# Kernel tuning notes

Hardware: AMD Instinct MI355X
Metric: run time of the kernel (lower is better)

The kernel has to match this reference:

```python
import jax, jax.numpy as jnp
import numpy as np

B, C, H, W = 8, 128, 256, 256
WS = 8          # window_size (square)
HEADS = 4


def setup_inputs() -> dict:
    key = jax.random.key(0)
    k1, k2, k3, k4 = jax.random.split(key, 4)
    x = jax.random.normal(k1, (B, C, H, W), dtype=jnp.float32)
    # 1x1 convs are per-pixel matmuls; store weights as [out, in]
    w_qkv = jax.random.normal(k2, (3 * C, C), dtype=jnp.float32) * 0.05   # qkv conv, bias=False
    w_proj = jax.random.normal(k3, (C, C), dtype=jnp.float32) * 0.05      # proj conv weight
    b_proj = jax.random.normal(k4, (C,), dtype=jnp.float32) * 0.01        # proj conv bias
    return {"x": x, "w_qkv": w_qkv, "w_proj": w_proj, "b_proj": b_proj}


def reference(x, w_qkv, w_proj, b_proj):
    b, c, h, w = x.shape
    ws, heads = WS, HEADS
    d = c // heads
    scale = d ** -0.5
    hn, wn = h // ws, w // ws
    n = ws * ws  # tokens per window

    # unfold with kernel=stride=ws -> row-major window partition
    # [B,C,H,W] -> [B*hn*wn, C, n]
    xw = x.reshape(b, c, hn, ws, wn, ws)
    xw = xw.transpose(0, 2, 4, 1, 3, 5).reshape(b * hn * wn, c, n)

    # 1x1 conv QKV projection (no bias)
    qkv = jnp.einsum('oc,bcn->bon', w_qkv, xw)  # [Bw, 3C, n]
    q, k, v = jnp.split(qkv, 3, axis=1)
    q = q.reshape(-1, heads, d, n)
    k = k.reshape(-1, heads, d, n)
    v = v.reshape(-1, heads, d, n)

    # attn = (q^T k) * scale, softmax over keys
    attn = jax.nn.softmax(jnp.einsum('bhdn,bhdm->bhnm', q, k) * scale, axis=-1)
    out = jnp.einsum('bhnm,bhdm->bhdn', attn, v).reshape(-1, c, n)  # [Bw, C, n]

    # 1x1 proj conv with bias
    out = jnp.einsum('oc,bcn->bon', w_proj, out) + b_proj[None, :, None]

    # fold windows back: [Bw, C, n] -> [B, C, H, W]
    out = out.reshape(b, hn, wn, c, ws, ws)
    out = out.transpose(0, 3, 1, 4, 2, 5).reshape(b, c, h, w)
    return out
```

## Files before the change

### kernel.cpp

```cpp
#include <hip/hip_runtime.h>


#define HH    256
#define WWID  256
#define SCALE 0.17677669529663687f
#define LOG2E 1.44269504088896340736f

typedef float  f32x4  __attribute__((ext_vector_type(4)));
typedef __bf16 bf16x8 __attribute__((ext_vector_type(8)));
typedef __bf16 bf16x4 __attribute__((ext_vector_type(4)));
typedef __bf16 bf16x2 __attribute__((ext_vector_type(2)));

#define SCR_BASE 16384

__global__ void prep_weights(const float* __restrict__ wqkv,
                             const float* __restrict__ wproj,
                             __bf16* __restrict__ wbf) {
  int i = blockIdx.x * 256 + threadIdx.x;
  float v = (i < 49152) ? wqkv[i] : wproj[i - 49152];
  if (i < 16384) v *= SCALE * LOG2E;
  wbf[i] = (__bf16)v;
}

__global__ __launch_bounds__(256, 2)
void winattn_main(const float* __restrict__ x,
                  const __bf16* __restrict__ wqkv,
                  const __bf16* __restrict__ wproj,
                  const float* __restrict__ bproj,
                  float* __restrict__ out) {
  __shared__ __align__(16) char smem[32768];

  const int tid  = threadIdx.x;
  const int lane = tid & 63;
  const int wv   = tid >> 6;
  const int l15  = lane & 15;
  const int l4   = lane >> 4;

  const int bid = blockIdx.x;
  const int win = ((bid & 7) << 10) | (bid >> 3);
  const int b   = win >> 10;
  const int wy  = (win >> 5) & 31;
  const int wx  = win & 31;
  const int gy0 = wy * 8, gx0 = wx * 8;

  #pragma unroll
  for (int it = 0; it < 4; ++it) {
    int idx   = tid + it * 256;
    int cpair = idx >> 4;
    int r     = idx & 15;
    int ty    = r >> 1, tx4 = r & 1;
    const float* px = x + (((size_t)(b * 128 + 2 * cpair) * HH + gy0 + ty) * WWID + gx0 + tx4 * 4);
    float4 v0 = *(const float4*)px;
    float4 v1 = *(const float4*)(px + (size_t)HH * WWID);
    float a0[4] = {v0.x, v0.y, v0.z, v0.w};
    float a1[4] = {v1.x, v1.y, v1.z, v1.w};
    #pragma unroll
    for (int i = 0; i < 4; ++i) {
      int tok = ty * 8 + tx4 * 4 + i;
      bf16x2 w2 = {(__bf16)a0[i], (__bf16)a1[i]};
      int byte = (tok * 256 + cpair * 4) ^ ((tok & 15) << 4);
      *(bf16x2*)(smem + byte) = w2;
    }
  }
  __syncthreads();

  const int scr = SCR_BASE + wv * 4096;
  bf16x8 bk[4], aq[4], bv[2][2];

  #define XT_AFRAG(mt, kt) \
    (*(const bf16x8*)(smem + ((((mt) * 16 + l15) * 256 + ((kt) * 32 + l4 * 8) * 2) ^ \
                              ((((mt) * 16 + l15) & 15) << 4))))

  {
    f32x4 accQ[2][4] = {}, accK[2][4] = {};
    __builtin_amdgcn_s_setprio(1);
    #pragma unroll
    for (int kt = 0; kt < 4; ++kt) {
      bf16x8 xf[4];
      #pragma unroll
      for (int mt = 0; mt < 4; ++mt) xf[mt] = XT_AFRAG(mt, kt);
      #pragma unroll
      for (int nt2 = 0; nt2 < 2; ++nt2) {
        bf16x8 wq = *(const bf16x8*)(wqkv + (size_t)(wv * 32 + nt2 * 16 + l15) * 128 + kt * 32 + l4 * 8);
        bf16x8 wk = *(const bf16x8*)(wqkv + (size_t)(128 + wv * 32 + nt2 * 16 + l15) * 128 + kt * 32 + l4 * 8);
        #pragma unroll
        for (int mt = 0; mt < 4; ++mt) {
          accQ[nt2][mt] = __builtin_amdgcn_mfma_f32_16x16x32_bf16(wq, xf[mt], accQ[nt2][mt], 0, 0, 0);
          accK[nt2][mt] = __builtin_amdgcn_mfma_f32_16x16x32_bf16(wk, xf[mt], accK[nt2][mt], 0, 0, 0);
        }
      }
    }
    __builtin_amdgcn_s_setprio(0);
    #pragma unroll
    for (int nt2 = 0; nt2 < 2; ++nt2)
      #pragma unroll
      for (int mt = 0; mt < 4; ++mt) {
        int tok = mt * 16 + l15;
        bf16x4 kp = {(__bf16)accK[nt2][mt][0], (__bf16)accK[nt2][mt][1],
                     (__bf16)accK[nt2][mt][2], (__bf16)accK[nt2][mt][3]};
        int byte = scr + ((tok * 64 + (nt2 * 16 + l4 * 4) * 2) ^ ((tok & 3) << 4));
        *(bf16x4*)(smem + byte) = kp;
      }
    #pragma unroll
    for (int mtS = 0; mtS < 4; ++mtS) {
      int m    = mtS * 16 + l15;
      int byte = scr + ((m * 64 + l4 * 16) ^ ((m & 3) << 4));
      bk[mtS] = *(const bf16x8*)(smem + byte);
    }
    #pragma unroll
    for (int nt2 = 0; nt2 < 2; ++nt2)
      #pragma unroll
      for (int mt = 0; mt < 4; ++mt) {
        int tok = mt * 16 + l15;
        bf16x4 qp = {(__bf16)accQ[nt2][mt][0], (__bf16)accQ[nt2][mt][1],
                     (__bf16)accQ[nt2][mt][2], (__bf16)accQ[nt2][mt][3]};
        int byte = scr + ((tok * 64 + (nt2 * 16 + l4 * 4) * 2) ^ ((tok & 3) << 4));
        *(bf16x4*)(smem + byte) = qp;
      }
    #pragma unroll
    for (int t = 0; t < 4; ++t) {
      int tok  = t * 16 + l15;
      int byte = scr + ((tok * 64 + l4 * 16) ^ ((tok & 3) << 4));
      aq[t] = *(const bf16x8*)(smem + byte);
    }
  }

  {
    f32x4 accV[2][4] = {};
    __builtin_amdgcn_s_setprio(1);
    #pragma unroll
    for (int kt = 0; kt < 4; ++kt) {
      bf16x8 xf[4];
      #pragma unroll
      for (int mt = 0; mt < 4; ++mt) xf[mt] = XT_AFRAG(mt, kt);
      #pragma unroll
      for (int nt2 = 0; nt2 < 2; ++nt2) {
        bf16x8 wf = *(const bf16x8*)(wqkv + (size_t)(256 + wv * 32 + nt2 * 16 + l15) * 128 + kt * 32 + l4 * 8);
        #pragma unroll
        for (int mt = 0; mt < 4; ++mt)
          accV[nt2][mt] = __builtin_amdgcn_mfma_f32_16x16x32_bf16(xf[mt], wf, accV[nt2][mt], 0, 0, 0);
      }
    }
    __builtin_amdgcn_s_setprio(0);
    #pragma unroll
    for (int nt2 = 0; nt2 < 2; ++nt2) {
      int dloc = nt2 * 16 + l15;
      #pragma unroll
      for (int mt = 0; mt < 4; ++mt) {
        int tok0 = mt * 16 + l4 * 4;
        bf16x4 vp = {(__bf16)accV[nt2][mt][0], (__bf16)accV[nt2][mt][1],
                     (__bf16)accV[nt2][mt][2], (__bf16)accV[nt2][mt][3]};
        int byte = scr + ((dloc * 128 + tok0 * 2) ^ ((dloc & 7) << 4));
        *(bf16x4*)(smem + byte) = vp;
      }
    }
    #pragma unroll
    for (int vt = 0; vt < 2; ++vt)
      #pragma unroll
      for (int kt = 0; kt < 2; ++kt) {
        int d    = vt * 16 + l15;
        int byte = scr + ((d * 128 + (kt * 32 + l4 * 8) * 2) ^ ((d & 7) << 4));
        bv[vt][kt] = *(const bf16x8*)(smem + byte);
      }
  }

  f32x4 oacc[2][2][2] = {};
  #pragma unroll
  for (int hf = 0; hf < 2; ++hf) {
    #pragma unroll
    for (int qt = 0; qt < 2; ++qt) {
      f32x4 st[4];
      __builtin_amdgcn_s_setprio(1);
      #pragma unroll
      for (int mtS = 0; mtS < 4; ++mtS) {
        f32x4 z = {0.f, 0.f, 0.f, 0.f};
        st[mtS] = __builtin_amdgcn_mfma_f32_16x16x32_bf16(bk[mtS], aq[hf * 2 + qt], z, 0, 0, 0);
      }
      __builtin_amdgcn_s_setprio(0);
      float mx = st[0][0];
      #pragma unroll
      for (int mtS = 0; mtS < 4; ++mtS)
        #pragma unroll
        for (int r = 0; r < 4; ++r) mx = fmaxf(mx, st[mtS][r]);
      mx = fmaxf(mx, __shfl_xor(mx, 16));
      mx = fmaxf(mx, __shfl_xor(mx, 32));
      float p[4][4];
      float sm = 0.f;
      #pragma unroll
      for (int mtS = 0; mtS < 4; ++mtS)
        #pragma unroll
        for (int r = 0; r < 4; ++r) {
          p[mtS][r] = __builtin_amdgcn_exp2f(st[mtS][r] - mx);
          sm += p[mtS][r];
        }
      sm += __shfl_xor(sm, 16);
      sm += __shfl_xor(sm, 32);
      float inv = __builtin_amdgcn_rcpf(sm);
      int qrow = qt * 16 + l15;
      int sw   = (qrow & 7) << 4;
      #pragma unroll
      for (int mtS = 0; mtS < 4; ++mtS) {
        bf16x4 pp = {(__bf16)(p[mtS][0] * inv), (__bf16)(p[mtS][1] * inv),
                     (__bf16)(p[mtS][2] * inv), (__bf16)(p[mtS][3] * inv)};
        int byte = scr + ((qrow * 128 + (mtS * 16 + l4 * 4) * 2) ^ sw);
        *(bf16x4*)(smem + byte) = pp;
      }
    }
    __builtin_amdgcn_s_setprio(1);
    #pragma unroll
    for (int kt = 0; kt < 2; ++kt)
      #pragma unroll
      for (int rt = 0; rt < 2; ++rt) {
        int nl   = rt * 16 + l15;
        int byte = scr + ((nl * 128 + (kt * 32 + l4 * 8) * 2) ^ ((nl & 7) << 4));
        bf16x8 ap = *(const bf16x8*)(smem + byte);
        #pragma unroll
        for (int vt = 0; vt < 2; ++vt)
          oacc[hf][rt][vt] =
              __builtin_amdgcn_mfma_f32_16x16x32_bf16(ap, bv[vt][kt], oacc[hf][rt][vt], 0, 0, 0);
      }
    __builtin_amdgcn_s_setprio(0);
  }
  __syncthreads();

  #pragma unroll
  for (int hf = 0; hf < 2; ++hf)
    #pragma unroll
    for (int rt = 0; rt < 2; ++rt)
      #pragma unroll
      for (int vt = 0; vt < 2; ++vt)
        #pragma unroll
        for (int r = 0; r < 4; ++r) {
          int tok  = hf * 32 + rt * 16 + l4 * 4 + r;
          int c    = wv * 32 + vt * 16 + l15;
          int byte = (tok * 256 + c * 2) ^ ((tok & 15) << 4);
          *(__bf16*)(smem + byte) = (__bf16)oacc[hf][rt][vt][r];
        }
  __syncthreads();

  f32x4 pacc[2][4] = {};
  __builtin_amdgcn_s_setprio(1);
  #pragma unroll
  for (int kt = 0; kt < 4; ++kt) {
    bf16x8 of[4];
    #pragma unroll
    for (int mt = 0; mt < 4; ++mt) of[mt] = XT_AFRAG(mt, kt);
    #pragma unroll
    for (int i = 0; i < 2; ++i) {
      bf16x8 wp = *(const bf16x8*)(wproj + (size_t)((wv * 2 + i) * 16 + l15) * 128 + kt * 32 + l4 * 8);
      #pragma unroll
      for (int mt = 0; mt < 4; ++mt)
        pacc[i][mt] = __builtin_amdgcn_mfma_f32_16x16x32_bf16(of[mt], wp, pacc[i][mt], 0, 0, 0);
    }
  }
  __builtin_amdgcn_s_setprio(0);

  #pragma unroll
  for (int i = 0; i < 2; ++i) {
    int o = (wv * 2 + i) * 16 + l15;
    float bias = bproj[o];
    float* obase = out + (size_t)(b * 128 + o) * ((size_t)HH * WWID) + gy0 * WWID + gx0;
    #pragma unroll
    for (int mt = 0; mt < 4; ++mt) {
      int tok0 = mt * 16 + l4 * 4;
      int ty = tok0 >> 3, tx0 = tok0 & 7;
      float4 f = {pacc[i][mt][0] + bias, pacc[i][mt][1] + bias,
                  pacc[i][mt][2] + bias, pacc[i][mt][3] + bias};
      *(float4*)(obase + ty * WWID + tx0) = f;
    }
  }
}

extern "C" void kernel_launch(void* const* d_in, const int* in_sizes, int n_in,
                              void* d_out, int out_size, void* d_ws, size_t ws_size,
                              hipStream_t stream) {
  const float* x     = (const float*)d_in[0];
  const float* wqkv  = (const float*)d_in[1];
  const float* wproj = (const float*)d_in[2];
  const float* bproj = (const float*)d_in[3];
  float* out = (float*)d_out;

  __bf16* wbf = (__bf16*)d_ws;
  prep_weights<<<256, 256, 0, stream>>>(wqkv, wproj, wbf);
  winattn_main<<<8192, 256, 0, stream>>>(x, wbf, wbf + 49152, bproj, out);
}
```

Before: 244.3 us.

## Keep Q/K/V and P in registers via 16x16x16 MFMA, dropping LDS round-trips

Q, K, V and the softmax probabilities now stay in registers. The MFMA accumulator outputs are packed to bf16 and fed directly as operands of 16x16x16 bf16 MFMAs, which replace the per-wave LDS scratch transposes and their reloads. This removes the LDS traffic and waits between the QKV projection, QK^T and PV stages, at the cost of twice as many smaller MFMA instructions. It also removes the s_setprio hints and enlarges the shared-memory declaration to 40960 bytes, which may reduce how many blocks fit per CU.

```diff
diff --git a/kernel.cpp b/kernel.cpp
--- a/kernel.cpp
+++ b/kernel.cpp
@@ -10,8 +10,23 @@
 typedef __bf16 bf16x8 __attribute__((ext_vector_type(8)));
 typedef __bf16 bf16x4 __attribute__((ext_vector_type(4)));
 typedef __bf16 bf16x2 __attribute__((ext_vector_type(2)));
-
-#define SCR_BASE 16384
+typedef short  s16x4  __attribute__((ext_vector_type(4)));
+
+__device__ __forceinline__ s16x4 pack4(f32x4 v) {
+  bf16x4 b = {(__bf16)v[0], (__bf16)v[1], (__bf16)v[2], (__bf16)v[3]};
+  return __builtin_bit_cast(s16x4, b);
+}
+
+#if __has_builtin(__builtin_amdgcn_mfma_f32_16x16x16bf16_1k)
+__device__ __forceinline__ f32x4 mfma16(s16x4 a, s16x4 b, f32x4 c) {
+  return __builtin_amdgcn_mfma_f32_16x16x16bf16_1k(a, b, c, 0, 0, 0);
+}
+#else
+__device__ __forceinline__ f32x4 mfma16(s16x4 a, s16x4 b, f32x4 c) {
+  asm("v_mfma_f32_16x16x16_bf16 %0, %1, %2, %0" : "+v"(c) : "v"(a), "v"(b));
+  return c;
+}
+#endif
 
 __global__ void prep_weights(const float* __restrict__ wqkv,
                              const float* __restrict__ wproj,
@@ -28,7 +43,7 @@
                   const __bf16* __restrict__ wproj,
                   const float* __restrict__ bproj,
                   float* __restrict__ out) {
-  __shared__ __align__(16) char smem[32768];
+  __shared__ __align__(16) char smem[40960];
 
   const int tid  = threadIdx.x;
   const int lane = tid & 63;
@@ -64,16 +79,13 @@
   }
   __syncthreads();
 
-  const int scr = SCR_BASE + wv * 4096;
-  bf16x8 bk[4], aq[4], bv[2][2];
-
   #define XT_AFRAG(mt, kt) \
     (*(const bf16x8*)(smem + ((((mt) * 16 + l15) * 256 + ((kt) * 32 + l4 * 8) * 2) ^ \
                               ((((mt) * 16 + l15) & 15) << 4))))
 
+  s16x4 qb[2][4], kb[2][4];
   {
     f32x4 accQ[2][4] = {}, accK[2][4] = {};
-    __builtin_amdgcn_s_setprio(1);
     #pragma unroll
     for (int kt = 0; kt < 4; ++kt) {
       bf16x8 xf[4];
@@ -90,44 +102,18 @@
         }
       }
     }
-    __builtin_amdgcn_s_setprio(0);
     #pragma unroll
     for (int nt2 = 0; nt2 < 2; ++nt2)
       #pragma unroll
       for (int mt = 0; mt < 4; ++mt) {
-        int tok = mt * 16 + l15;
-        bf16x4 kp = {(__bf16)accK[nt2][mt][0], (__bf16)accK[nt2][mt][1],
-                     (__bf16)accK[nt2][mt][2], (__bf16)accK[nt2][mt][3]};
-        int byte = scr + ((tok * 64 + (nt2 * 16 + l4 * 4) * 2) ^ ((tok & 3) << 4));
-        *(bf16x4*)(smem + byte) = kp;
-      }
-    #pragma unroll
-    for (int mtS = 0; mtS < 4; ++mtS) {
-      int m    = mtS * 16 + l15;
-      int byte = scr + ((m * 64 + l4 * 16) ^ ((m & 3) << 4));
-      bk[mtS] = *(const bf16x8*)(smem + byte);
-    }
-    #pragma unroll
-    for (int nt2 = 0; nt2 < 2; ++nt2)
-      #pragma unroll
-      for (int mt = 0; mt < 4; ++mt) {
-        int tok = mt * 16 + l15;
-        bf16x4 qp = {(__bf16)accQ[nt2][mt][0], (__bf16)accQ[nt2][mt][1],
-                     (__bf16)accQ[nt2][mt][2], (__bf16)accQ[nt2][mt][3]};
-        int byte = scr + ((tok * 64 + (nt2 * 16 + l4 * 4) * 2) ^ ((tok & 3) << 4));
-        *(bf16x4*)(smem + byte) = qp;
-      }
-    #pragma unroll
-    for (int t = 0; t < 4; ++t) {
-      int tok  = t * 16 + l15;
-      int byte = scr + ((tok * 64 + l4 * 16) ^ ((tok & 3) << 4));
-      aq[t] = *(const bf16x8*)(smem + byte);
-    }
-  }
-
+        qb[nt2][mt] = pack4(accQ[nt2][mt]);
+        kb[nt2][mt] = pack4(accK[nt2][mt]);
+      }
+  }
+
+  s16x4 vb[2][4];
   {
     f32x4 accV[2][4] = {};
-    __builtin_amdgcn_s_setprio(1);
     #pragma unroll
     for (int kt = 0; kt < 4; ++kt) {
       bf16x8 xf[4];
@@ -141,105 +127,69 @@
           accV[nt2][mt] = __builtin_amdgcn_mfma_f32_16x16x32_bf16(xf[mt], wf, accV[nt2][mt], 0, 0, 0);
       }
     }
-    __builtin_amdgcn_s_setprio(0);
-    #pragma unroll
-    for (int nt2 = 0; nt2 < 2; ++nt2) {
-      int dloc = nt2 * 16 + l15;
-      #pragma unroll
-      for (int mt = 0; mt < 4; ++mt) {
-        int tok0 = mt * 16 + l4 * 4;
-        bf16x4 vp = {(__bf16)accV[nt2][mt][0], (__bf16)accV[nt2][mt][1],
-                     (__bf16)accV[nt2][mt][2], (__bf16)accV[nt2][mt][3]};
-        int byte = scr + ((dloc * 128 + tok0 * 2) ^ ((dloc & 7) << 4));
-        *(bf16x4*)(smem + byte) = vp;
-      }
-    }
-    #pragma unroll
-    for (int vt = 0; vt < 2; ++vt)
-      #pragma unroll
-      for (int kt = 0; kt < 2; ++kt) {
-        int d    = vt * 16 + l15;
-        int byte = scr + ((d * 128 + (kt * 32 + l4 * 8) * 2) ^ ((d & 7) << 4));
-        bv[vt][kt] = *(const bf16x8*)(smem + byte);
-      }
-  }
-
-  f32x4 oacc[2][2][2] = {};
-  #pragma unroll
-  for (int hf = 0; hf < 2; ++hf) {
-    #pragma unroll
-    for (int qt = 0; qt < 2; ++qt) {
-      f32x4 st[4];
-      __builtin_amdgcn_s_setprio(1);
-      #pragma unroll
-      for (int mtS = 0; mtS < 4; ++mtS) {
-        f32x4 z = {0.f, 0.f, 0.f, 0.f};
-        st[mtS] = __builtin_amdgcn_mfma_f32_16x16x32_bf16(bk[mtS], aq[hf * 2 + qt], z, 0, 0, 0);
-      }
-      __builtin_amdgcn_s_setprio(0);
-      float mx = st[0][0];
-      #pragma unroll
-      for (int mtS = 0; mtS < 4; ++mtS)
-        #pragma unroll
-        for (int r = 0; r < 4; ++r) mx = fmaxf(mx, st[mtS][r]);
-      mx = fmaxf(mx, __shfl_xor(mx, 16));
-      mx = fmaxf(mx, __shfl_xor(mx, 32));
-      float p[4][4];
-      float sm = 0.f;
-      #pragma unroll
-      for (int mtS = 0; mtS < 4; ++mtS)
-        #pragma unroll
-        for (int r = 0; r < 4; ++r) {
-          p[mtS][r] = __builtin_amdgcn_exp2f(st[mtS][r] - mx);
-          sm += p[mtS][r];
-        }
-      sm += __shfl_xor(sm, 16);
-      sm += __shfl_xor(sm, 32);
-      float inv = __builtin_amdgcn_rcpf(sm);
-      int qrow = qt * 16 + l15;
-      int sw   = (qrow & 7) << 4;
-      #pragma unroll
-      for (int mtS = 0; mtS < 4; ++mtS) {
-        bf16x4 pp = {(__bf16)(p[mtS][0] * inv), (__bf16)(p[mtS][1] * inv),
-                     (__bf16)(p[mtS][2] * inv), (__bf16)(p[mtS][3] * inv)};
-        int byte = scr + ((qrow * 128 + (mtS * 16 + l4 * 4) * 2) ^ sw);
-        *(bf16x4*)(smem + byte) = pp;
-      }
-    }
-    __builtin_amdgcn_s_setprio(1);
-    #pragma unroll
-    for (int kt = 0; kt < 2; ++kt)
-      #pragma unroll
-      for (int rt = 0; rt < 2; ++rt) {
-        int nl   = rt * 16 + l15;
-        int byte = scr + ((nl * 128 + (kt * 32 + l4 * 8) * 2) ^ ((nl & 7) << 4));
-        bf16x8 ap = *(const bf16x8*)(smem + byte);
-        #pragma unroll
-        for (int vt = 0; vt < 2; ++vt)
-          oacc[hf][rt][vt] =
-              __builtin_amdgcn_mfma_f32_16x16x32_bf16(ap, bv[vt][kt], oacc[hf][rt][vt], 0, 0, 0);
-      }
-    __builtin_amdgcn_s_setprio(0);
+    #pragma unroll
+    for (int nt2 = 0; nt2 < 2; ++nt2)
+      #pragma unroll
+      for (int mt = 0; mt < 4; ++mt) vb[nt2][mt] = pack4(accV[nt2][mt]);
+  }
+
+  f32x4 oacc[4][2] = {};
+  #pragma unroll
+  for (int t = 0; t < 4; ++t) {
+    f32x4 st[4];
+    #pragma unroll
+    for (int m = 0; m < 4; ++m) {
+      f32x4 z = {0.f, 0.f, 0.f, 0.f};
+      st[m] = mfma16(kb[0][m], qb[0][t], z);
+      st[m] = mfma16(kb[1][m], qb[1][t], st[m]);
+    }
+    float mx = st[0][0];
+    #pragma unroll
+    for (int m = 0; m < 4; ++m)
+      #pragma unroll
+      for (int r = 0; r < 4; ++r) mx = fmaxf(mx, st[m][r]);
+    mx = fmaxf(mx, __shfl_xor(mx, 16));
+    mx = fmaxf(mx, __shfl_xor(mx, 32));
+    float p[4][4];
+    float sm = 0.f;
+    #pragma unroll
+    for (int m = 0; m < 4; ++m)
+      #pragma unroll
+      for (int r = 0; r < 4; ++r) {
+        p[m][r] = __builtin_amdgcn_exp2f(st[m][r] - mx);
+        sm += p[m][r];
+      }
+    sm += __shfl_xor(sm, 16);
+    sm += __shfl_xor(sm, 32);
+    float inv = __builtin_amdgcn_rcpf(sm);
+    s16x4 ap[4];
+    #pragma unroll
+    for (int m = 0; m < 4; ++m) {
+      f32x4 pn = {p[m][0] * inv, p[m][1] * inv, p[m][2] * inv, p[m][3] * inv};
+      ap[m] = pack4(pn);
+    }
+    #pragma unroll
+    for (int m = 0; m < 4; ++m)
+      #pragma unroll
+      for (int n = 0; n < 2; ++n)
+        oacc[t][n] = mfma16(ap[m], vb[n][m], oacc[t][n]);
   }
   __syncthreads();
 
   #pragma unroll
-  for (int hf = 0; hf < 2; ++hf)
-    #pragma unroll
-    for (int rt = 0; rt < 2; ++rt)
-      #pragma unroll
-      for (int vt = 0; vt < 2; ++vt)
-        #pragma unroll
-        for (int r = 0; r < 4; ++r) {
-          int tok  = hf * 32 + rt * 16 + l4 * 4 + r;
-          int c    = wv * 32 + vt * 16 + l15;
-          int byte = (tok * 256 + c * 2) ^ ((tok & 15) << 4);
-          *(__bf16*)(smem + byte) = (__bf16)oacc[hf][rt][vt][r];
-        }
+  for (int t = 0; t < 4; ++t)
+    #pragma unroll
+    for (int n = 0; n < 2; ++n)
+      #pragma unroll
+      for (int r = 0; r < 4; ++r) {
+        int tok  = t * 16 + l4 * 4 + r;
+        int c    = wv * 32 + n * 16 + l15;
+        int byte = (tok * 256 + c * 2) ^ ((tok & 15) << 4);
+        *(__bf16*)(smem + byte) = (__bf16)oacc[t][n][r];
+      }
   __syncthreads();
 
   f32x4 pacc[2][4] = {};
-  __builtin_amdgcn_s_setprio(1);
   #pragma unroll
   for (int kt = 0; kt < 4; ++kt) {
     bf16x8 of[4];
@@ -253,7 +203,6 @@
         pacc[i][mt] = __builtin_amdgcn_mfma_f32_16x16x32_bf16(of[mt], wp, pacc[i][mt], 0, 0, 0);
     }
   }
-  __builtin_amdgcn_s_setprio(0);
 
   #pragma unroll
   for (int i = 0; i < 2; ++i) {
```

New measurement: 262.7 us. +7.5%, slower.
